# Kernel optimization log

Hardware: AMD Instinct MI355X
Metric: run time of the kernel (lower is better)

The kernel has to match this reference:

```python
import jax, jax.numpy as jnp
import numpy as np

B = 65536   # batch
S = 3       # pad_size / seq len
DIN = 72    # input feature dim
D = 100     # dim_model
H = 10      # num_head
DH = D // H # dim_head = 10
FF = 512    # ffn hidden
L = 8       # encoder layers
CLS = 40    # cls_dim


def _pos_encoding():
    pe = np.array([[pos / 10000.0 ** (i // 2 * 2.0 / D) for i in range(D)]
                   for pos in range(S)], dtype=np.float32)
    pe[:, 0::2] = np.sin(pe[:, 0::2])
    pe[:, 1::2] = np.cos(pe[:, 1::2])
    return jnp.asarray(pe)  # [S, D]


def setup_inputs() -> dict:
    key = jax.random.key(0)
    ks = jax.random.split(key, 24)
    n = lambda k, shape: 0.05 * jax.random.normal(k, shape, dtype=jnp.float32)
    inp = {
        'x': jax.random.normal(ks[0], (B, S, DIN), dtype=jnp.float32),
        'label': jax.random.randint(ks[1], (B,), 0, CLS),
        'fa_label': jax.random.randint(ks[2], (B,), 0, CLS),
        'We': n(ks[3], (D, DIN)), 'be': n(ks[4], (D,)),
        'pe': _pos_encoding(),
        'Wq': n(ks[5], (L, D, D)), 'bq': n(ks[6], (L, D)),
        'Wk': n(ks[7], (L, D, D)), 'bk': n(ks[8], (L, D)),
        'Wv': n(ks[9], (L, D, D)), 'bv': n(ks[10], (L, D)),
        'Wo': n(ks[11], (L, D, D)), 'bo': n(ks[12], (L, D)),
        'ln1_g': jnp.ones((L, D), jnp.float32), 'ln1_b': jnp.zeros((L, D), jnp.float32),
        'W1': n(ks[13], (L, FF, D)), 'b1': n(ks[14], (L, FF)),
        'W2': n(ks[15], (L, D, FF)), 'b2': n(ks[16], (L, D)),
        'ln2_g': jnp.ones((L, D), jnp.float32), 'ln2_b': jnp.zeros((L, D), jnp.float32),
        'Wf': n(ks[17], (CLS, S * D)), 'bf': n(ks[18], (CLS,)),
    }
    return inp


def _ln(x, g, b, eps=1e-5):
    m = x.mean(-1, keepdims=True)
    v = ((x - m) ** 2).mean(-1, keepdims=True)
    return (x - m) / jnp.sqrt(v + eps) * g + b


def _forward(x, We, be, pe, Wq, bq, Wk, bk, Wv, bv, Wo, bo,
             ln1_g, ln1_b, W1, b1, W2, b2, ln2_g, ln2_b, Wf, bf):
    Bsz = x.shape[0]
    out = x @ We.T + be          # [B, S, D] embedding
    out = out + pe               # positional encoding (dropout = identity in eval)
    scale = DH ** -0.5
    for i in range(L):
        xin = out
        Q = xin @ Wq[i].T + bq[i]
        K = xin @ Wk[i].T + bk[i]
        V = xin @ Wv[i].T + bv[i]
        # Faithful row-major reshape (original uses .view, which interleaves
        # seq and head dims rather than a transpose-based head split).
        Qh = Q.reshape(Bsz * H, -1, DH)   # [B*H, S, DH]
        Kh = K.reshape(Bsz * H, -1, DH)
        Vh = V.reshape(Bsz * H, -1, DH)
        attn = jax.nn.softmax(jnp.einsum('bqd,bkd->bqk', Qh, Kh) * scale, axis=-1)
        ctx = jnp.einsum('bqk,bkd->bqd', attn, Vh).reshape(Bsz, -1, D)
        out = _ln(ctx @ Wo[i].T + bo[i] + xin, ln1_g[i], ln1_b[i])
        # position-wise FFN
        h = jax.nn.relu(out @ W1[i].T + b1[i])
        out = _ln(h @ W2[i].T + b2[i] + out, ln2_g[i], ln2_b[i])
    out = out.reshape(Bsz, S * D) @ Wf.T + bf   # [B, CLS]
    return out


def reference(x, label, fa_label, We, be, pe, Wq, bq, Wk, bk, Wv, bv, Wo, bo,
              ln1_g, ln1_b, W1, b1, W2, b2, ln2_g, ln2_b, Wf, bf):
    # label / fa_label are unused in the original forward
    return _forward(x, We, be, pe, Wq, bq, Wk, bk, Wv, bv, Wo, bo,
                    ln1_g, ln1_b, W1, b1, W2, b2, ln2_g, ln2_b, Wf, bf)
```

## Files before the change

kernel.cpp:

```cpp
#include <hip/hip_runtime.h>
#include <hip/hip_bf16.h>


typedef __attribute__((ext_vector_type(8))) short short8;
typedef __attribute__((ext_vector_type(4))) float floatx4;

namespace {
constexpr int S = 3, DIN = 72, D = 100, FF = 512, L = 8, CLS = 40;
constexpr int NB = 16, R = 48, NT = 256;
constexpr int LDA = 136;
constexpr int LDH = 264;
constexpr int LDV = 100;
constexpr float SCALE = 0.3162277660168379f;

constexpr int PL_QKVO = 7 * 4 * 512;
constexpr int WQ_OFF = 0;
constexpr int WK_OFF = WQ_OFF + L * PL_QKVO;
constexpr int WV_OFF = WK_OFF + L * PL_QKVO;
constexpr int WO_OFF = WV_OFF + L * PL_QKVO;
constexpr int PL_W1 = 32 * 4 * 512;
constexpr int W1_OFF = WO_OFF + L * PL_QKVO;
constexpr int PL_W2 = 7 * 16 * 512;
constexpr int W2_OFF = W1_OFF + L * PL_W1;
constexpr int WE_OFF = W2_OFF + L * PL_W2;
}

__device__ __forceinline__ unsigned short f2bf(float f) {
  unsigned int u = __float_as_uint(f);
  u = u + 0x7fffu + ((u >> 16) & 1u);
  return (unsigned short)(u >> 16);
}

__device__ __forceinline__ unsigned pkbf(float a, float b) {
  __hip_bfloat162 h = __float22bfloat162_rn(make_float2(a, b));
  return *reinterpret_cast<unsigned*>(&h);
}

__device__ __forceinline__ void st_bf4(unsigned short* p, floatx4 v) {
  *reinterpret_cast<uint2*>(p) = make_uint2(pkbf(v.x, v.y), pkbf(v.z, v.w));
}

__device__ __forceinline__ void load10(float* o, const unsigned short* p) {
  const unsigned* u = (const unsigned*)p;
#pragma unroll
  for (int w = 0; w < 5; ++w) {
    unsigned x = u[w];
    o[2 * w] = __uint_as_float(x << 16);
    o[2 * w + 1] = __uint_as_float(x & 0xffff0000u);
  }
}

__device__ __forceinline__ void ldwf4(const unsigned short* base, short8* o) {
#pragma unroll
  for (int ks = 0; ks < 4; ++ks) o[ks] = *(const short8*)(base + ks * 512);
}

__device__ __forceinline__ void owner_ln(floatx4* M, const float* scrRow,
                                         const float* __restrict__ g,
                                         const float* __restrict__ b,
                                         unsigned short* sARow, int ln_o,
                                         int cnt) {
  floatx4 v[7];
  float sum = 0.f;
#pragma unroll
  for (int i = 0; i < 7; ++i)
    if (i < cnt) {
      const int col = i * 16 + ln_o * 4;
      floatx4 t = M[i] + *(const floatx4*)(scrRow + col);
      v[i] = t;
      sum += t.x + t.y + t.z + t.w;
    }
  sum += __shfl_xor(sum, 1, 4);
  sum += __shfl_xor(sum, 2, 4);
  const float mean = sum * 0.01f;
  float var = 0.f;
#pragma unroll
  for (int i = 0; i < 7; ++i)
    if (i < cnt) {
      floatx4 d = v[i] - mean;
      var += d.x * d.x + d.y * d.y + d.z * d.z + d.w * d.w;
    }
  var += __shfl_xor(var, 1, 4);
  var += __shfl_xor(var, 2, 4);
  const float rstd = rsqrtf(var * 0.01f + 1e-5f);
#pragma unroll
  for (int i = 0; i < 7; ++i)
    if (i < cnt) {
      const int col = i * 16 + ln_o * 4;
      floatx4 o = (v[i] - mean) * rstd * *(const floatx4*)(g + col) +
                  *(const floatx4*)(b + col);
      M[i] = o;
      st_bf4(sARow + col, o);
    }
}

__global__ void prep_weights(const float* __restrict__ Wq, const float* __restrict__ Wk,
                             const float* __restrict__ Wv, const float* __restrict__ Wo,
                             const float* __restrict__ W1, const float* __restrict__ W2,
                             const float* __restrict__ We,
                             unsigned short* __restrict__ ws) {
  const int gid = blockIdx.x * 256 + threadIdx.x;
  constexpr int T_QKVO = 8 * 7 * 4 * 64;
  constexpr int T_W1 = 8 * 32 * 4 * 64;
  constexpr int T_W2 = 8 * 7 * 16 * 64;
  constexpr int T_WE = 7 * 3 * 64;
  if (gid >= 4 * T_QKVO + T_W1 + T_W2 + T_WE) return;

  const float* src;
  unsigned short* dst;
  int within, ntc, ksc, N, Ksrc, lstride;
  if (gid < 4 * T_QKVO) {
    const int t = gid / T_QKVO;
    within = gid % T_QKVO;
    src = (t == 0 ? Wq : t == 1 ? Wk : t == 2 ? Wv : Wo);
    dst = ws + (t == 0 ? WQ_OFF : t == 1 ? WK_OFF : t == 2 ? WV_OFF : WO_OFF);
    ntc = 7; ksc = 4; N = 100; Ksrc = 100; lstride = 10000;
  } else if (gid < 4 * T_QKVO + T_W1) {
    within = gid - 4 * T_QKVO;
    src = W1; dst = ws + W1_OFF;
    ntc = 32; ksc = 4; N = 512; Ksrc = 100; lstride = 51200;
  } else if (gid < 4 * T_QKVO + T_W1 + T_W2) {
    within = gid - 4 * T_QKVO - T_W1;
    src = W2; dst = ws + W2_OFF;
    ntc = 7; ksc = 16; N = 100; Ksrc = 512; lstride = 51200;
  } else {
    within = gid - 4 * T_QKVO - T_W1 - T_W2;
    src = We; dst = ws + WE_OFF;
    ntc = 7; ksc = 3; N = 100; Ksrc = 72; lstride = 0;
  }
  const int lane = within & 63;
  int tmp = within >> 6;
  const int ks = tmp % ksc; tmp /= ksc;
  const int nt = tmp % ntc;
  const int lay = tmp / ntc;
  const int n = nt * 16 + (lane & 15);
  const int kb = ks * 32 + (lane >> 4) * 8;
  const float* sp = src + (size_t)lay * lstride + (size_t)n * Ksrc;
  unsigned short o[8];
#pragma unroll
  for (int j = 0; j < 8; ++j) {
    const int k = kb + j;
    float v = (n < N && k < Ksrc) ? sp[k] : 0.f;
    o[j] = f2bf(v);
  }
  uint4 pk = make_uint4((unsigned)o[0] | ((unsigned)o[1] << 16),
                        (unsigned)o[2] | ((unsigned)o[3] << 16),
                        (unsigned)o[4] | ((unsigned)o[5] << 16),
                        (unsigned)o[6] | ((unsigned)o[7] << 16));
  *reinterpret_cast<uint4*>(dst + (size_t)within * 8) = pk;
}

__global__ __launch_bounds__(NT, 3)
void geomap_mfma(const float* __restrict__ gx,
                 const float* __restrict__ be, const float* __restrict__ pe,
                 const float* __restrict__ bq, const float* __restrict__ bk,
                 const float* __restrict__ bv, const float* __restrict__ bo,
                 const float* __restrict__ g1, const float* __restrict__ bt1,
                 const float* __restrict__ b1, const float* __restrict__ b2,
                 const float* __restrict__ g2, const float* __restrict__ bt2,
                 const float* __restrict__ Wf, const float* __restrict__ bfc,
                 const unsigned short* __restrict__ ws,
                 float* __restrict__ gout) {
  __shared__ __align__(16) char smem[41856];
  unsigned short* sA = (unsigned short*)smem;
  unsigned short* sQ = (unsigned short*)(smem + 13056);
  unsigned short* sK = (unsigned short*)(smem + 22656);
  unsigned short* sV = (unsigned short*)(smem + 32256);
  unsigned short* sH = (unsigned short*)(smem + 13056);
  float* scr = (float*)(smem + 13056);

  const int tid = threadIdx.x;
  const int lane = tid & 63;
  const int wid = tid >> 6;
  const int l15 = lane & 15;
  const int quad = lane >> 4;
  const int blk = blockIdx.x;

  const bool owner = tid < 192;
  const int row_o = tid >> 2, ln_o = tid & 3;
  const int cnt_o = (ln_o == 0) ? 7 : 6;
  floatx4 M[7];

  for (int i = tid; i < R * LDA / 2; i += NT) ((unsigned*)sA)[i] = 0u;
  __syncthreads();
  for (int i = tid; i < R * DIN / 2; i += NT) {
    const int row = i / 36, c = (i % 36) * 2;
    const float2 f2 = *(const float2*)(gx + ((size_t)blk * R + row) * DIN + c);
    ((unsigned*)sA)[row * (LDA / 2) + (c >> 1)] = pkbf(f2.x, f2.y);
  }
  __syncthreads();

  {
    short8 xe[3][3];
#pragma unroll
    for (int mt = 0; mt < 3; ++mt)
#pragma unroll
      for (int ks = 0; ks < 3; ++ks)
        xe[mt][ks] = *(const short8*)(sA + (mt * 16 + l15) * LDA + ks * 32 + quad * 8);
    __syncthreads();
    for (int nt = wid; nt < 7; nt += 4) {
      const unsigned short* wb = ws + WE_OFF + (size_t)(nt * 3) * 512 + (size_t)lane * 8;
      short8 w0 = *(const short8*)(wb);
      short8 w1 = *(const short8*)(wb + 512);
      short8 w2 = *(const short8*)(wb + 1024);
      const int n0 = nt * 16 + quad * 4;
      floatx4 a[3];
#pragma unroll
      for (int mt = 0; mt < 3; ++mt) {
        a[mt] = floatx4{0.f, 0.f, 0.f, 0.f};
        a[mt] = __builtin_amdgcn_mfma_f32_16x16x32_bf16(w0, xe[mt][0], a[mt], 0, 0, 0);
        a[mt] = __builtin_amdgcn_mfma_f32_16x16x32_bf16(w1, xe[mt][1], a[mt], 0, 0, 0);
        a[mt] = __builtin_amdgcn_mfma_f32_16x16x32_bf16(w2, xe[mt][2], a[mt], 0, 0, 0);
      }
      if (n0 < D) {
        const floatx4 bev = *(const floatx4*)(be + n0);
#pragma unroll
        for (int mt = 0; mt < 3; ++mt) {
          const int row = mt * 16 + l15;
          const int s = row % 3;
          const floatx4 pev = *(const floatx4*)(pe + s * D + n0);
          const floatx4 o = a[mt] + bev + pev;
          *(floatx4*)(scr + row * D + n0) = o;
          st_bf4(sA + row * LDA + n0, o);
        }
      }
    }
  }
  __syncthreads();
  if (owner) {
#pragma unroll
    for (int i = 0; i < 7; ++i)
      if (i < cnt_o) M[i] = *(const floatx4*)(scr + row_o * D + i * 16 + ln_o * 4);
  }
  __syncthreads();

  for (int lay = 0; lay < L; ++lay) {
    {
      short8 xf[3][4];
#pragma unroll
      for (int mt = 0; mt < 3; ++mt)
#pragma unroll
        for (int ks = 0; ks < 4; ++ks)
          xf[mt][ks] = *(const short8*)(sA + (mt * 16 + l15) * LDA + ks * 32 + quad * 8);
      const unsigned short* wbase[3] = {ws + WQ_OFF + lay * PL_QKVO,
                                        ws + WK_OFF + lay * PL_QKVO,
                                        ws + WV_OFF + lay * PL_QKVO};
      short8 wf[4];
      ldwf4(wbase[wid / 7] + (size_t)(wid % 7) * 2048 + (size_t)lane * 8, wf);
      for (int u = wid; u < 21; u += 4) {
        short8 nwf[4];
        const bool more = (u + 4 < 21);
        if (more)
          ldwf4(wbase[(u + 4) / 7] + (size_t)((u + 4) % 7) * 2048 + (size_t)lane * 8, nwf);
        const int mat = u / 7, nt = u % 7;
        const int n0 = nt * 16 + quad * 4;
        floatx4 bias = {0.f, 0.f, 0.f, 0.f};
        const float* bsrc = (mat == 0 ? bq : mat == 1 ? bk : bv) + lay * D;
        if (n0 < D) bias = *(const floatx4*)(bsrc + n0);
        floatx4 a0 = bias, a1 = bias, a2 = bias;
#pragma unroll
        for (int ks = 0; ks < 4; ++ks) {
          a0 = __builtin_amdgcn_mfma_f32_16x16x32_bf16(wf[ks], xf[0][ks], a0, 0, 0, 0);
          a1 = __builtin_amdgcn_mfma_f32_16x16x32_bf16(wf[ks], xf[1][ks], a1, 0, 0, 0);
          a2 = __builtin_amdgcn_mfma_f32_16x16x32_bf16(wf[ks], xf[2][ks], a2, 0, 0, 0);
        }
        if (n0 < D) {
          const floatx4 av[3] = {a0, a1, a2};
#pragma unroll
          for (int mt = 0; mt < 3; ++mt) {
            const int row = mt * 16 + l15;
            if (mat == 0) st_bf4(sQ + row * 100 + n0, av[mt]);
            else if (mat == 1) st_bf4(sK + row * 100 + n0, av[mt]);
            else {
              unsigned* dp = (unsigned*)(sV + row * LDV + n0);
              dp[0] = pkbf(av[mt].x, av[mt].y);
              dp[1] = pkbf(av[mt].z, av[mt].w);
            }
          }
        }
#pragma unroll
        for (int ks = 0; ks < 4; ++ks) wf[ks] = more ? nwf[ks] : wf[ks];
      }
    }
    __syncthreads();

    if (tid < 160) {
      const int e = tid / 10, h = tid % 10;
      const unsigned short* Qe = sQ + e * 300;
      const unsigned short* Ke = sK + e * 300;
      const unsigned short* Ve = sV + e * 300;
      float K[3][10], V[3][10];
#pragma unroll
      for (int t = 0; t < 3; ++t) {
        load10(K[t], Ke + h * 30 + t * 10);
        load10(V[t], Ve + h * 30 + t * 10);
      }
#pragma unroll
      for (int sq = 0; sq < 3; ++sq) {
        float q[10];
        load10(q, Qe + h * 30 + sq * 10);
        float sc[3];
#pragma unroll
        for (int t = 0; t < 3; ++t) {
          float s0 = 0.f;
#pragma unroll
          for (int j = 0; j < 10; ++j) s0 += q[j] * K[t][j];
          sc[t] = s0 * SCALE;
        }
        const float m = fmaxf(sc[0], fmaxf(sc[1], sc[2]));
        float p0 = __expf(sc[0] - m), p1 = __expf(sc[1] - m), p2 = __expf(sc[2] - m);
        const float inv = 1.f / (p0 + p1 + p2);
        p0 *= inv; p1 *= inv; p2 *= inv;
        float ctx[10];
#pragma unroll
        for (int j = 0; j < 10; ++j)
          ctx[j] = p0 * V[0][j] + p1 * V[1][j] + p2 * V[2][j];
        const int p = h * 30 + sq * 10;
        unsigned* dp = (unsigned*)(sA + (e * 3 + p / 100) * LDA + (p % 100));
#pragma unroll
        for (int w = 0; w < 5; ++w) dp[w] = pkbf(ctx[2 * w], ctx[2 * w + 1]);
      }
    }
    __syncthreads();

    {
      short8 cf[3][4];
#pragma unroll
      for (int mt = 0; mt < 3; ++mt)
#pragma unroll
        for (int ks = 0; ks < 4; ++ks)
          cf[mt][ks] = *(const short8*)(sA + (mt * 16 + l15) * LDA + ks * 32 + quad * 8);
      const unsigned short* wbase = ws + WO_OFF + lay * PL_QKVO;
      short8 wf[4];
      ldwf4(wbase + (size_t)wid * 2048 + (size_t)lane * 8, wf);
      for (int u = wid; u < 7; u += 4) {
        short8 nwf[4];
        const bool more = (u + 4 < 7);
        if (more) ldwf4(wbase + (size_t)(u + 4) * 2048 + (size_t)lane * 8, nwf);
        const int n0 = u * 16 + quad * 4;
        floatx4 bias = {0.f, 0.f, 0.f, 0.f};
        if (n0 < D) bias = *(const floatx4*)(bo + lay * D + n0);
        floatx4 a0 = bias, a1 = bias, a2 = bias;
#pragma unroll
        for (int ks = 0; ks < 4; ++ks) {
          a0 = __builtin_amdgcn_mfma_f32_16x16x32_bf16(wf[ks], cf[0][ks], a0, 0, 0, 0);
          a1 = __builtin_amdgcn_mfma_f32_16x16x32_bf16(wf[ks], cf[1][ks], a1, 0, 0, 0);
          a2 = __builtin_amdgcn_mfma_f32_16x16x32_bf16(wf[ks], cf[2][ks], a2, 0, 0, 0);
        }
        if (n0 < D) {
          const floatx4 av[3] = {a0, a1, a2};
#pragma unroll
          for (int mt = 0; mt < 3; ++mt)
            *(floatx4*)(scr + (mt * 16 + l15) * D + n0) = av[mt];
        }
#pragma unroll
        for (int ks = 0; ks < 4; ++ks) wf[ks] = more ? nwf[ks] : wf[ks];
      }
    }
    __syncthreads();
    if (owner)
      owner_ln(M, scr + row_o * D, g1 + lay * D, bt1 + lay * D,
               sA + row_o * LDA, ln_o, cnt_o);
    __syncthreads();

    {
      short8 ff[3][4];
#pragma unroll
      for (int mt = 0; mt < 3; ++mt)
#pragma unroll
        for (int ks = 0; ks < 4; ++ks)
          ff[mt][ks] = *(const short8*)(sA + (mt * 16 + l15) * LDA + ks * 32 + quad * 8);
      floatx4 facc[2][3];
#pragma unroll
      for (int idx = 0; idx < 2; ++idx) {
        const int nt = wid + 4 * idx;
        const int n0 = nt * 16 + quad * 4;
        floatx4 bias = {0.f, 0.f, 0.f, 0.f};
        if (nt < 7 && n0 < D) bias = *(const floatx4*)(b2 + lay * D + n0);
#pragma unroll
        for (int mt = 0; mt < 3; ++mt) facc[idx][mt] = bias;
      }
      const unsigned short* w1b = ws + W1_OFF + (size_t)lay * PL_W1;
      const unsigned short* w2b = ws + W2_OFF + (size_t)lay * PL_W2;
      const int nts1 = wid + 4;

      for (int c = 0; c < 2; ++c) {
        short8 wf[4];
        ldwf4(w1b + (size_t)(c * 16 + wid) * 2048 + (size_t)lane * 8, wf);
#pragma unroll
        for (int k = 0; k < 4; ++k) {
          const int ntg = c * 16 + wid + 4 * k;
          short8 nwf[4];
          if (k < 3)
            ldwf4(w1b + (size_t)(ntg + 4) * 2048 + (size_t)lane * 8, nwf);
          const floatx4 b1v = *(const floatx4*)(b1 + lay * FF + ntg * 16 + quad * 4);
          floatx4 a0 = b1v, a1 = b1v, a2 = b1v;
#pragma unroll
          for (int ks = 0; ks < 4; ++ks) {
            a0 = __builtin_amdgcn_mfma_f32_16x16x32_bf16(wf[ks], ff[0][ks], a0, 0, 0, 0);
            a1 = __builtin_amdgcn_mfma_f32_16x16x32_bf16(wf[ks], ff[1][ks], a1, 0, 0, 0);
            a2 = __builtin_amdgcn_mfma_f32_16x16x32_bf16(wf[ks], ff[2][ks], a2, 0, 0, 0);
          }
          const int nloc = (wid + 4 * k) * 16 + quad * 4;
          const floatx4 av[3] = {a0, a1, a2};
#pragma unroll
          for (int mt = 0; mt < 3; ++mt) {
            const int row = mt * 16 + l15;
            floatx4 r;
            r.x = fmaxf(av[mt].x, 0.f); r.y = fmaxf(av[mt].y, 0.f);
            r.z = fmaxf(av[mt].z, 0.f); r.w = fmaxf(av[mt].w, 0.f);
            st_bf4(sH + row * LDH + nloc, r);
          }
          if (k < 3) {
#pragma unroll
            for (int ks = 0; ks < 4; ++ks) wf[ks] = nwf[ks];
          }
        }
        __syncthreads();
        short8 wA = *(const short8*)(w2b + (size_t)(wid * 16 + c * 8) * 512 + (size_t)lane * 8);
        short8 wB = wA;
        if (nts1 < 7)
          wB = *(const short8*)(w2b + (size_t)(nts1 * 16 + c * 8) * 512 + (size_t)lane * 8);
#pragma unroll
        for (int ksl = 0; ksl < 8; ++ksl) {
          short8 nA = wA, nB = wB;
          if (ksl < 7) {
            nA = *(const short8*)(w2b + (size_t)(wid * 16 + c * 8 + ksl + 1) * 512 + (size_t)lane * 8);
            if (nts1 < 7)
              nB = *(const short8*)(w2b + (size_t)(nts1 * 16 + c * 8 + ksl + 1) * 512 + (size_t)lane * 8);
          }
          short8 hf[3];
#pragma unroll
          for (int mt = 0; mt < 3; ++mt)
            hf[mt] = *(const short8*)(sH + (mt * 16 + l15) * LDH + ksl * 32 + quad * 8);
#pragma unroll
          for (int mt = 0; mt < 3; ++mt)
            facc[0][mt] = __builtin_amdgcn_mfma_f32_16x16x32_bf16(wA, hf[mt], facc[0][mt], 0, 0, 0);
          if (nts1 < 7) {
#pragma unroll
            for (int mt = 0; mt < 3; ++mt)
              facc[1][mt] = __builtin_amdgcn_mfma_f32_16x16x32_bf16(wB, hf[mt], facc[1][mt], 0, 0, 0);
          }
          wA = nA; wB = nB;
        }
        __syncthreads();
      }
#pragma unroll
      for (int idx = 0; idx < 2; ++idx) {
        const int nt = wid + 4 * idx;
        const int n0 = nt * 16 + quad * 4;
        if (nt < 7 && n0 < D) {
#pragma unroll
          for (int mt = 0; mt < 3; ++mt)
            *(floatx4*)(scr + (mt * 16 + l15) * D + n0) = facc[idx][mt];
        }
      }
    }
    __syncthreads();
    if (owner)
      owner_ln(M, scr + row_o * D, g2 + lay * D, bt2 + lay * D,
               sA + row_o * LDA, ln_o, cnt_o);
    __syncthreads();
  }

  if (owner) {
#pragma unroll
    for (int i = 0; i < 7; ++i)
      if (i < cnt_o)
        *(floatx4*)(scr + row_o * D + i * 16 + ln_o * 4) = M[i];
  }
  __syncthreads();
  if (tid < 160) {
    const int c = tid % 40, eg = tid / 40;
    float acc[4];
#pragma unroll
    for (int i = 0; i < 4; ++i) acc[i] = bfc[c];
    const floatx4* wr = (const floatx4*)(Wf + c * 300);
    for (int kq = 0; kq < 75; ++kq) {
      const floatx4 w4 = wr[kq];
#pragma unroll
      for (int i = 0; i < 4; ++i) {
        const floatx4 x4 = *(const floatx4*)(scr + (eg * 4 + i) * 300 + kq * 4);
        acc[i] += w4.x * x4.x + w4.y * x4.y + w4.z * x4.z + w4.w * x4.w;
      }
    }
#pragma unroll
    for (int i = 0; i < 4; ++i)
      gout[((size_t)blk * NB + eg * 4 + i) * CLS + c] = acc[i];
  }
}

extern "C" void kernel_launch(void* const* d_in, const int* in_sizes, int n_in,
                              void* d_out, int out_size, void* d_ws,
                              size_t ws_size, hipStream_t stream) {
  const float* x   = (const float*)d_in[0];
  const float* We  = (const float*)d_in[3];
  const float* be  = (const float*)d_in[4];
  const float* pe  = (const float*)d_in[5];
  const float* Wq  = (const float*)d_in[6];
  const float* bq  = (const float*)d_in[7];
  const float* Wk  = (const float*)d_in[8];
  const float* bk  = (const float*)d_in[9];
  const float* Wv  = (const float*)d_in[10];
  const float* bv  = (const float*)d_in[11];
  const float* Wo  = (const float*)d_in[12];
  const float* bo  = (const float*)d_in[13];
  const float* g1  = (const float*)d_in[14];
  const float* bt1 = (const float*)d_in[15];
  const float* W1  = (const float*)d_in[16];
  const float* b1  = (const float*)d_in[17];
  const float* W2  = (const float*)d_in[18];
  const float* b2  = (const float*)d_in[19];
  const float* g2  = (const float*)d_in[20];
  const float* bt2 = (const float*)d_in[21];
  const float* Wf  = (const float*)d_in[22];
  const float* bf  = (const float*)d_in[23];
  float* out = (float*)d_out;
  unsigned short* ws = (unsigned short*)d_ws;

  prep_weights<<<710, 256, 0, stream>>>(Wq, Wk, Wv, Wo, W1, W2, We, ws);

  const int B = in_sizes[0] / (S * DIN);
  const int blocks = B / NB;
  geomap_mfma<<<blocks, 256, 0, stream>>>(x, be, pe, bq, bk, bv, bo,
                                          g1, bt1, b1, b2, g2, bt2, Wf, bf,
                                          ws, out);
}
```

Before: 1.474 ms.

## Store V in the activation buffer and drop weight prefetch to raise occupancy

The V projection now writes into the sA activation buffer, after an added barrier once X fragments are loaded into registers. This drops the separate sV shared-memory region and shrinks LDS per block. Attention is restructured to compute all softmax probabilities first, then read V from sA and overwrite it with ctx. The software-pipelined next-tile weight prefetch registers are removed from the QKV, O and W1 loops, and launch bounds go from 3 to 4 blocks per CU, trading latency hiding for occupancy.

Measured after the change: 1.627 ms. +10.4%, slower.

```diff
diff --git a/kernel.cpp b/kernel.cpp
--- a/kernel.cpp
+++ b/kernel.cpp
@@ -10,7 +10,6 @@
 constexpr int NB = 16, R = 48, NT = 256;
 constexpr int LDA = 136;
 constexpr int LDH = 264;
-constexpr int LDV = 100;
 constexpr float SCALE = 0.3162277660168379f;
 
 constexpr int PL_QKVO = 7 * 4 * 512;
@@ -150,7 +149,7 @@
   *reinterpret_cast<uint4*>(dst + (size_t)within * 8) = pk;
 }
 
-__global__ __launch_bounds__(NT, 3)
+__global__ __launch_bounds__(NT, 4)
 void geomap_mfma(const float* __restrict__ gx,
                  const float* __restrict__ be, const float* __restrict__ pe,
                  const float* __restrict__ bq, const float* __restrict__ bk,
@@ -161,11 +160,10 @@
                  const float* __restrict__ Wf, const float* __restrict__ bfc,
                  const unsigned short* __restrict__ ws,
                  float* __restrict__ gout) {
-  __shared__ __align__(16) char smem[41856];
+  __shared__ __align__(16) char smem[38400];
   unsigned short* sA = (unsigned short*)smem;
   unsigned short* sQ = (unsigned short*)(smem + 13056);
   unsigned short* sK = (unsigned short*)(smem + 22656);
-  unsigned short* sV = (unsigned short*)(smem + 32256);
   unsigned short* sH = (unsigned short*)(smem + 13056);
   float* scr = (float*)(smem + 13056);
 
@@ -242,17 +240,14 @@
 #pragma unroll
         for (int ks = 0; ks < 4; ++ks)
           xf[mt][ks] = *(const short8*)(sA + (mt * 16 + l15) * LDA + ks * 32 + quad * 8);
+      __syncthreads();
       const unsigned short* wbase[3] = {ws + WQ_OFF + lay * PL_QKVO,
                                         ws + WK_OFF + lay * PL_QKVO,
                                         ws + WV_OFF + lay * PL_QKVO};
-      short8 wf[4];
-      ldwf4(wbase[wid / 7] + (size_t)(wid % 7) * 2048 + (size_t)lane * 8, wf);
       for (int u = wid; u < 21; u += 4) {
-        short8 nwf[4];
-        const bool more = (u + 4 < 21);
-        if (more)
-          ldwf4(wbase[(u + 4) / 7] + (size_t)((u + 4) % 7) * 2048 + (size_t)lane * 8, nwf);
         const int mat = u / 7, nt = u % 7;
+        short8 wf[4];
+        ldwf4(wbase[mat] + (size_t)nt * 2048 + (size_t)lane * 8, wf);
         const int n0 = nt * 16 + quad * 4;
         floatx4 bias = {0.f, 0.f, 0.f, 0.f};
         const float* bsrc = (mat == 0 ? bq : mat == 1 ? bk : bv) + lay * D;
@@ -271,15 +266,9 @@
             const int row = mt * 16 + l15;
             if (mat == 0) st_bf4(sQ + row * 100 + n0, av[mt]);
             else if (mat == 1) st_bf4(sK + row * 100 + n0, av[mt]);
-            else {
-              unsigned* dp = (unsigned*)(sV + row * LDV + n0);
-              dp[0] = pkbf(av[mt].x, av[mt].y);
-              dp[1] = pkbf(av[mt].z, av[mt].w);
-            }
+            else st_bf4(sA + row * LDA + n0, av[mt]);
           }
         }
-#pragma unroll
-        for (int ks = 0; ks < 4; ++ks) wf[ks] = more ? nwf[ks] : wf[ks];
       }
     }
     __syncthreads();
@@ -288,13 +277,10 @@
       const int e = tid / 10, h = tid % 10;
       const unsigned short* Qe = sQ + e * 300;
       const unsigned short* Ke = sK + e * 300;
-      const unsigned short* Ve = sV + e * 300;
-      float K[3][10], V[3][10];
-#pragma unroll
-      for (int t = 0; t < 3; ++t) {
-        load10(K[t], Ke + h * 30 + t * 10);
-        load10(V[t], Ve + h * 30 + t * 10);
-      }
+      float Kv[3][10];
+#pragma unroll
+      for (int t = 0; t < 3; ++t) load10(Kv[t], Ke + h * 30 + t * 10);
+      float p[3][3];
 #pragma unroll
       for (int sq = 0; sq < 3; ++sq) {
         float q[10];
@@ -304,21 +290,36 @@
         for (int t = 0; t < 3; ++t) {
           float s0 = 0.f;
 #pragma unroll
-          for (int j = 0; j < 10; ++j) s0 += q[j] * K[t][j];
+          for (int j = 0; j < 10; ++j) s0 += q[j] * Kv[t][j];
           sc[t] = s0 * SCALE;
         }
         const float m = fmaxf(sc[0], fmaxf(sc[1], sc[2]));
         float p0 = __expf(sc[0] - m), p1 = __expf(sc[1] - m), p2 = __expf(sc[2] - m);
         const float inv = 1.f / (p0 + p1 + p2);
-        p0 *= inv; p1 *= inv; p2 *= inv;
-        float ctx[10];
-#pragma unroll
-        for (int j = 0; j < 10; ++j)
-          ctx[j] = p0 * V[0][j] + p1 * V[1][j] + p2 * V[2][j];
-        const int p = h * 30 + sq * 10;
-        unsigned* dp = (unsigned*)(sA + (e * 3 + p / 100) * LDA + (p % 100));
-#pragma unroll
-        for (int w = 0; w < 5; ++w) dp[w] = pkbf(ctx[2 * w], ctx[2 * w + 1]);
+        p[sq][0] = p0 * inv; p[sq][1] = p1 * inv; p[sq][2] = p2 * inv;
+      }
+      float ctx[3][10];
+#pragma unroll
+      for (int sq = 0; sq < 3; ++sq)
+#pragma unroll
+        for (int j = 0; j < 10; ++j) ctx[sq][j] = 0.f;
+#pragma unroll
+      for (int t = 0; t < 3; ++t) {
+        const int pv = h * 30 + t * 10;
+        float vv[10];
+        load10(vv, sA + (e * 3 + pv / 100) * LDA + (pv % 100));
+#pragma unroll
+        for (int sq = 0; sq < 3; ++sq)
+#pragma unroll
+          for (int j = 0; j < 10; ++j) ctx[sq][j] += p[sq][t] * vv[j];
+      }
+#pragma unroll
+      for (int sq = 0; sq < 3; ++sq) {
+        const int pq = h * 30 + sq * 10;
+        unsigned* dp = (unsigned*)(sA + (e * 3 + pq / 100) * LDA + (pq % 100));
+#pragma unroll
+        for (int w = 0; w < 5; ++w)
+          dp[w] = pkbf(ctx[sq][2 * w], ctx[sq][2 * w + 1]);
       }
     }
     __syncthreads();
@@ -331,12 +332,9 @@
         for (int ks = 0; ks < 4; ++ks)
           cf[mt][ks] = *(const short8*)(sA + (mt * 16 + l15) * LDA + ks * 32 + quad * 8);
       const unsigned short* wbase = ws + WO_OFF + lay * PL_QKVO;
-      short8 wf[4];
-      ldwf4(wbase + (size_t)wid * 2048 + (size_t)lane * 8, wf);
       for (int u = wid; u < 7; u += 4) {
-        short8 nwf[4];
-        const bool more = (u + 4 < 7);
-        if (more) ldwf4(wbase + (size_t)(u + 4) * 2048 + (size_t)lane * 8, nwf);
+        short8 wf[4];
+        ldwf4(wbase + (size_t)u * 2048 + (size_t)lane * 8, wf);
         const int n0 = u * 16 + quad * 4;
         floatx4 bias = {0.f, 0.f, 0.f, 0.f};
         if (n0 < D) bias = *(const floatx4*)(bo + lay * D + n0);
@@ -353,8 +351,6 @@
           for (int mt = 0; mt < 3; ++mt)
             *(floatx4*)(scr + (mt * 16 + l15) * D + n0) = av[mt];
         }
-#pragma unroll
-        for (int ks = 0; ks < 4; ++ks) wf[ks] = more ? nwf[ks] : wf[ks];
       }
     }
     __syncthreads();
@@ -385,14 +381,11 @@
       const int nts1 = wid + 4;
 
       for (int c = 0; c < 2; ++c) {
-        short8 wf[4];
-        ldwf4(w1b + (size_t)(c * 16 + wid) * 2048 + (size_t)lane * 8, wf);
 #pragma unroll
         for (int k = 0; k < 4; ++k) {
           const int ntg = c * 16 + wid + 4 * k;
-          short8 nwf[4];
-          if (k < 3)
-            ldwf4(w1b + (size_t)(ntg + 4) * 2048 + (size_t)lane * 8, nwf);
+          short8 wf[4];
+          ldwf4(w1b + (size_t)ntg * 2048 + (size_t)lane * 8, wf);
           const floatx4 b1v = *(const floatx4*)(b1 + lay * FF + ntg * 16 + quad * 4);
           floatx4 a0 = b1v, a1 = b1v, a2 = b1v;
 #pragma unroll
@@ -410,10 +403,6 @@
             r.x = fmaxf(av[mt].x, 0.f); r.y = fmaxf(av[mt].y, 0.f);
             r.z = fmaxf(av[mt].z, 0.f); r.w = fmaxf(av[mt].w, 0.f);
             st_bf4(sH + row * LDH + nloc, r);
-          }
-          if (k < 3) {
-#pragma unroll
-            for (int ks = 0; ks < 4; ++ks) wf[ks] = nwf[ks];
           }
         }
         __syncthreads();
```
